# Optimization experiments

Hardware: AMD Instinct MI355X
Metric: run time of the kernel (lower is better)

## Reference

```python
import jax, jax.numpy as jnp
import numpy as np


def _dft_mats(N1, N):
    # Symmetric N1xN1 DFT / iDFT matrices and Cooley-Tukey twiddle factors.
    n = np.arange(N1)
    F = np.exp(-2j * np.pi * np.outer(n, n) / N1).astype(np.complex64)
    Finv = np.conj(F)  # inverse DFT matrix (1/N normalization folded into tw)
    tw = (np.exp(-2j * np.pi * np.outer(n, n) / N) / N).astype(np.complex64)
    twinv = np.exp(2j * np.pi * np.outer(n, n) / N).astype(np.complex64)
    return F, Finv, tw, twinv


def setup_inputs() -> dict:
    key = jax.random.key(0)
    ku, kk = jax.random.split(key)
    B, H, N = 128, 128, 1024
    u = jax.random.normal(ku, (B, H, N), dtype=jnp.float32)
    k = jax.random.normal(kk, (H, N), dtype=jnp.float32)
    return {"u": u, "k": k}


def reference(u, k):
    # Four-step (Monarch / Cooley-Tukey) FFT convolution: y = ifft(fft(u) * fft(k)).real
    # decomposed into N1xN1 complex matmuls with twiddle multiplies, matching TKFFTConv.
    B, H, N = u.shape
    N1 = int(round(np.sqrt(N)))
    F, Finv, tw, twinv = map(jnp.asarray, _dft_mats(N1, N))

    # Filter spectrum, reshaped (k2, k1) then transposed -> (H, k1, k2), as in __init__.
    kf = jnp.fft.fft(k, n=N)                              # (H, N) complex64
    kfT = jnp.swapaxes(kf.reshape(H, N1, N1), -1, -2)     # (H, k1, k2)

    x = u.reshape(B, H, N1, N1).astype(jnp.complex64)     # (B, H, n1, n2)
    x = jnp.einsum('kn,bhnm->bhkm', F, x)                 # DFT over n1 -> (k1, n2)
    x = x * tw                                            # twiddle (includes 1/N)
    x = jnp.einsum('bhkn,nl->bhkl', x, F)                 # DFT over n2 -> (k1, k2)
    x = x * kfT[None]                                     # pointwise filter in freq
    x = jnp.einsum('bhkl,ln->bhkn', x, Finv)              # iDFT over k2 -> (k1, n2)
    x = x * twinv                                         # inverse twiddle
    x = jnp.einsum('nk,bhkm->bhnm', Finv, x)              # iDFT over k1 -> (n1, n2)
    return x.real.reshape(B, H, N)
```

## Files before the change

### kernel.cpp

```cpp
#include <hip/hip_runtime.h>
#include <hip/hip_bf16.h>
#include <math.h>

typedef __attribute__((ext_vector_type(8))) short short8;
typedef __attribute__((ext_vector_type(16))) float f32x16;

union U {
    unsigned u[4];
    short8 s;
};

struct FragH {
    U f[2];
};

static __device__ __forceinline__ unsigned short f2bf(float x) {
    __bf16 b = (__bf16)x;
    return __builtin_bit_cast(unsigned short, b);
}
static __device__ __forceinline__ unsigned packbf(float a, float b) {
    return (unsigned)f2bf(a) | ((unsigned)f2bf(b) << 16);
}

#define MFMA(A, B, C) __builtin_amdgcn_mfma_f32_32x32x16_bf16((A).s, (B).s, (C), 0, 0, 0)


__global__ __launch_bounds__(256) void fft_tables(float2* tabs, float2* T1, uint4* Ftab) {
    int gid = blockIdx.x * 256 + threadIdx.x;
    if (gid < 1024) {
        int i = gid;
        int r = i >> 5, c = i & 31;
        float s32, c32;
        sincospif((float)((r * c) & 31) / 16.0f, &s32, &c32);
        s32 = -s32;
        tabs[i]        = make_float2(c32,  s32);
        tabs[1024 + i] = make_float2(c32, -s32);
        float sN, cN;
        sincospif((float)(r * c) / 512.0f, &sN, &cN);
        sN = -sN;
        tabs[2048 + i] = make_float2(cN / 1024.0f, sN / 1024.0f);
        tabs[3072 + i] = make_float2(cN, -sN);
        int m = i >> 6, l = i & 63;
        int row = (m & 3) + 8 * (m >> 2) + 4 * (l >> 5);
        int prod = (l & 31) * row;
        float st, ct;
        sincospif((float)prod / 512.0f, &st, &ct);
        T1[i] = make_float2(ct, -st);
    }
    if (gid < 1536) {
        int c = gid >> 9;
        int rem = gid & 511;
        int t = rem >> 8;
        int sub = rem & 255;
        int l = sub >> 2;
        int v = sub & 3;
        int k0 = 16 * t + 8 * (l >> 5) + 2 * v;
        int j = l & 31;
        unsigned short sh[2];
        for (int q = 0; q < 2; q++) {
            int k = k0 + q;
            float sa, ca;
            sincospif((float)((k * j) & 31) / 16.0f, &sa, &ca);
            float base = (c == 0) ? ca : ((c == 1) ? -sa : sa);
            sh[q] = f2bf(base);
        }
        ((unsigned*)Ftab)[((c * 2 + t) * 64 + l) * 4 + v] =
            (unsigned)sh[0] | ((unsigned)sh[1] << 16);
    }
}

__global__ __launch_bounds__(256) void kf_kernel(const float* __restrict__ kin,
                                                 const float2* __restrict__ tabs,
                                                 float2* __restrict__ kf_cd) {
    __shared__ float  sx[1024];
    __shared__ float2 sA[1024];
    const int h = blockIdx.x, t = threadIdx.x;
    for (int i = t; i < 1024; i += 256) sx[i] = kin[h * 1024 + i];
    __syncthreads();
    const int r = t >> 3, c0 = (t & 7) << 2;

    float2 acc[4];
    for (int j = 0; j < 4; j++) acc[j] = make_float2(0.f, 0.f);
    #pragma unroll 8
    for (int n1 = 0; n1 < 32; n1++) {
        float2 f = tabs[r * 32 + n1];
        for (int j = 0; j < 4; j++) {
            float xv = sx[n1 * 32 + c0 + j];
            acc[j].x += f.x * xv;
            acc[j].y += f.y * xv;
        }
    }
    for (int j = 0; j < 4; j++) {
        float2 w = tabs[3072 + r * 32 + c0 + j];
        sA[r * 32 + c0 + j] = make_float2(acc[j].x * w.x + acc[j].y * w.y,
                                          acc[j].y * w.x - acc[j].x * w.y);
    }
    __syncthreads();
    for (int j = 0; j < 4; j++) acc[j] = make_float2(0.f, 0.f);
    #pragma unroll 8
    for (int n2 = 0; n2 < 32; n2++) {
        float2 a = sA[r * 32 + n2];
        for (int j = 0; j < 4; j++) {
            float2 f = tabs[n2 * 32 + c0 + j];
            acc[j].x += a.x * f.x - a.y * f.y;
            acc[j].y += a.x * f.y + a.y * f.x;
        }
    }
    for (int j = 0; j < 4; j++) {
        int k2 = c0 + j;
        int m = (k2 & 3) | ((k2 >> 3) << 2);
        int hl = (k2 >> 2) & 1;
        kf_cd[h * 1024 + m * 64 + hl * 32 + r] =
            make_float2(acc[j].x * (1.0f / 1024.0f), acc[j].y * (1.0f / 1024.0f));
    }
}

static __device__ __forceinline__ void convertP(const f32x16& acc, FragH& out) {
    #pragma unroll
    for (int t = 0; t < 2; t++) {
        unsigned a0 = packbf(acc[8 * t + 0], acc[8 * t + 1]);
        unsigned a1 = packbf(acc[8 * t + 2], acc[8 * t + 3]);
        unsigned b0 = packbf(acc[8 * t + 4], acc[8 * t + 5]);
        unsigned b1 = packbf(acc[8 * t + 6], acc[8 * t + 7]);
        asm("v_permlane32_swap_b32 %0, %1" : "+v"(a0), "+v"(b0));
        asm("v_permlane32_swap_b32 %0, %1" : "+v"(a1), "+v"(b1));
        out.f[t].u[0] = a0;
        out.f[t].u[1] = a1;
        out.f[t].u[2] = b0;
        out.f[t].u[3] = b1;
    }
}

__global__ __launch_bounds__(256, 3) void conv_mfma(const float* __restrict__ u,
                                                    const float2* __restrict__ T1,
                                                    const uint4* __restrict__ Ftab,
                                                    const float2* __restrict__ KF,
                                                    float* __restrict__ out) {
    __shared__ float  sIO[8 * 1024];
    __shared__ float2 sT1[1024];
    __shared__ float2 sKF[1024];

    const int tid = threadIdx.x;
    const int lane = tid & 63;
    const int wave = tid >> 6;
    const int col = lane & 31;
    const int hl = lane >> 5;

    const int h = blockIdx.x >> 4;
    const int bblk = (blockIdx.x & 15) * 8;

    #pragma unroll
    for (int j = 0; j < 8; j++) {
        const float4* src = (const float4*)(u + ((size_t)((bblk + j) * 128 + h) << 10));
        *(float4*)&sIO[j * 1024 + tid * 4] = src[tid];
    }
    for (int i = tid; i < 1024; i += 256) {
        sT1[i] = T1[i];
        sKF[i] = KF[h * 1024 + i];
    }

    U F[3][2];
    #pragma unroll
    for (int c = 0; c < 3; c++)
        #pragma unroll
        for (int t = 0; t < 2; t++) {
            uint4 raw = Ftab[(c * 2 + t) * 64 + lane];
            F[c][t].u[0] = raw.x; F[c][t].u[1] = raw.y;
            F[c][t].u[2] = raw.z; F[c][t].u[3] = raw.w;
        }
    __syncthreads();

    const int tR = wave * 2, tI = wave * 2 + 1;
    U Xr[2], Xi[2];
    #pragma unroll
    for (int t = 0; t < 2; t++)
        #pragma unroll
        for (int v = 0; v < 4; v++) {
            int r0 = (16 * t + 8 * hl + 2 * v) * 32 + col;
            Xr[t].u[v] = packbf(sIO[tR * 1024 + r0], sIO[tR * 1024 + r0 + 32]);
            Xi[t].u[v] = packbf(sIO[tI * 1024 + r0], sIO[tI * 1024 + r0 + 32]);
        }

    const f32x16 Z16 = {0,0,0,0,0,0,0,0,0,0,0,0,0,0,0,0};

    f32x16 aR = Z16, aI = Z16;
    #pragma unroll
    for (int t = 0; t < 2; t++) {
        aR = MFMA(Xr[t], F[0][t], aR); aR = MFMA(Xi[t], F[2][t], aR);
        aI = MFMA(Xr[t], F[1][t], aI); aI = MFMA(Xi[t], F[0][t], aI);
    }
    #pragma unroll
    for (int m = 0; m < 16; m++) {
        float2 tm = sT1[m * 64 + lane];
        float rr = aR[m] * tm.x - aI[m] * tm.y;
        float ii = aR[m] * tm.y + aI[m] * tm.x;
        aR[m] = rr; aI[m] = ii;
    }
    FragH Yr, Yi;
    convertP(aR, Yr);
    convertP(aI, Yi);

    f32x16 bR = Z16, bI = Z16;
    #pragma unroll
    for (int t = 0; t < 2; t++) {
        bR = MFMA(F[0][t], Yr.f[t], bR); bR = MFMA(F[2][t], Yi.f[t], bR);
        bI = MFMA(F[0][t], Yi.f[t], bI); bI = MFMA(F[1][t], Yr.f[t], bI);
    }
    #pragma unroll
    for (int m = 0; m < 16; m++) {
        float2 kv = sKF[m * 64 + lane];
        float rr = bR[m] * kv.x - bI[m] * kv.y;
        float ii = bR[m] * kv.y + bI[m] * kv.x;
        bR[m] = rr; bI[m] = ii;
    }
    FragH Zr, Zi;
    convertP(bR, Zr);
    convertP(bI, Zi);

    aR = Z16; aI = Z16;
    #pragma unroll
    for (int t = 0; t < 2; t++) {
        aR = MFMA(Zr.f[t], F[0][t], aR); aR = MFMA(Zi.f[t], F[1][t], aR);
        aI = MFMA(Zr.f[t], F[2][t], aI); aI = MFMA(Zi.f[t], F[0][t], aI);
    }
    #pragma unroll
    for (int m = 0; m < 16; m++) {
        float2 tm = sT1[m * 64 + lane];
        float rr = aR[m] * tm.x + aI[m] * tm.y;
        float ii = aI[m] * tm.x - aR[m] * tm.y;
        aR[m] = rr; aI[m] = ii;
    }
    FragH Wr, Wi;
    convertP(aR, Wr);
    convertP(aI, Wi);

    f32x16 yR = Z16, yI = Z16;
    #pragma unroll
    for (int t = 0; t < 2; t++) {
        yR = MFMA(F[0][t], Wr.f[t], yR); yR = MFMA(F[1][t], Wi.f[t], yR);
        yI = MFMA(F[0][t], Wi.f[t], yI); yI = MFMA(F[2][t], Wr.f[t], yI);
    }

    #pragma unroll
    for (int m = 0; m < 16; m++) {
        int off = ((m & 3) + 8 * (m >> 2) + 4 * hl) * 32 + col;
        sIO[tR * 1024 + off] = yR[m];
        sIO[tI * 1024 + off] = yI[m];
    }
    __syncthreads();

    #pragma unroll
    for (int j = 0; j < 8; j++) {
        float4* dst = (float4*)(out + ((size_t)((bblk + j) * 128 + h) << 10));
        dst[tid] = *(const float4*)&sIO[j * 1024 + tid * 4];
    }
}

extern "C" void kernel_launch(void* const* d_in, const int* in_sizes, int n_in,
                              void* d_out, int out_size, void* d_ws, size_t ws_size,
                              hipStream_t stream) {
    const float* u = (const float*)d_in[0];
    const float* k = (const float*)d_in[1];
    float* out = (float*)d_out;

    float2* tabs  = (float2*)d_ws;
    float2* T1    = (float2*)((char*)d_ws + 32768);
    uint4*  Ftab  = (uint4*)((char*)d_ws + 49152);
    float2* kf_cd = (float2*)((char*)d_ws + 65536);

    fft_tables<<<16, 256, 0, stream>>>(tabs, T1, Ftab);
    kf_kernel<<<128, 256, 0, stream>>>(k, tabs, kf_cd);
    conv_mfma<<<2048, 256, 0, stream>>>(u, T1, Ftab, kf_cd, out);
}
```

Measured before the change: 46.11 us.

## Fuse table generation and filter FFT into single conv kernel with direct global IO

Removes the separate table and filter-spectrum kernels: each block computes twiddles and DFT fragments with sincospif, and runs the filter FFT through MFMA in-kernel for its head. The main kernel drops the shared-memory staging buffer and reads and writes u/out directly from global memory in fragment layout, with each wave processing two batch pairs. This cuts two launches and shared-memory traffic, at the cost of redundant per-block trig and filter work, uncoalesced strided global accesses, and a bf16-precision filter spectrum.

```diff
diff --git a/kernel.cpp b/kernel.cpp
--- a/kernel.cpp
+++ b/kernel.cpp
@@ -23,97 +23,6 @@
 }
 
 #define MFMA(A, B, C) __builtin_amdgcn_mfma_f32_32x32x16_bf16((A).s, (B).s, (C), 0, 0, 0)
-
-
-__global__ __launch_bounds__(256) void fft_tables(float2* tabs, float2* T1, uint4* Ftab) {
-    int gid = blockIdx.x * 256 + threadIdx.x;
-    if (gid < 1024) {
-        int i = gid;
-        int r = i >> 5, c = i & 31;
-        float s32, c32;
-        sincospif((float)((r * c) & 31) / 16.0f, &s32, &c32);
-        s32 = -s32;
-        tabs[i]        = make_float2(c32,  s32);
-        tabs[1024 + i] = make_float2(c32, -s32);
-        float sN, cN;
-        sincospif((float)(r * c) / 512.0f, &sN, &cN);
-        sN = -sN;
-        tabs[2048 + i] = make_float2(cN / 1024.0f, sN / 1024.0f);
-        tabs[3072 + i] = make_float2(cN, -sN);
-        int m = i >> 6, l = i & 63;
-        int row = (m & 3) + 8 * (m >> 2) + 4 * (l >> 5);
-        int prod = (l & 31) * row;
-        float st, ct;
-        sincospif((float)prod / 512.0f, &st, &ct);
-        T1[i] = make_float2(ct, -st);
-    }
-    if (gid < 1536) {
-        int c = gid >> 9;
-        int rem = gid & 511;
-        int t = rem >> 8;
-        int sub = rem & 255;
-        int l = sub >> 2;
-        int v = sub & 3;
-        int k0 = 16 * t + 8 * (l >> 5) + 2 * v;
-        int j = l & 31;
-        unsigned short sh[2];
-        for (int q = 0; q < 2; q++) {
-            int k = k0 + q;
-            float sa, ca;
-            sincospif((float)((k * j) & 31) / 16.0f, &sa, &ca);
-            float base = (c == 0) ? ca : ((c == 1) ? -sa : sa);
-            sh[q] = f2bf(base);
-        }
-        ((unsigned*)Ftab)[((c * 2 + t) * 64 + l) * 4 + v] =
-            (unsigned)sh[0] | ((unsigned)sh[1] << 16);
-    }
-}
-
-__global__ __launch_bounds__(256) void kf_kernel(const float* __restrict__ kin,
-                                                 const float2* __restrict__ tabs,
-                                                 float2* __restrict__ kf_cd) {
-    __shared__ float  sx[1024];
-    __shared__ float2 sA[1024];
-    const int h = blockIdx.x, t = threadIdx.x;
-    for (int i = t; i < 1024; i += 256) sx[i] = kin[h * 1024 + i];
-    __syncthreads();
-    const int r = t >> 3, c0 = (t & 7) << 2;
-
-    float2 acc[4];
-    for (int j = 0; j < 4; j++) acc[j] = make_float2(0.f, 0.f);
-    #pragma unroll 8
-    for (int n1 = 0; n1 < 32; n1++) {
-        float2 f = tabs[r * 32 + n1];
-        for (int j = 0; j < 4; j++) {
-            float xv = sx[n1 * 32 + c0 + j];
-            acc[j].x += f.x * xv;
-            acc[j].y += f.y * xv;
-        }
-    }
-    for (int j = 0; j < 4; j++) {
-        float2 w = tabs[3072 + r * 32 + c0 + j];
-        sA[r * 32 + c0 + j] = make_float2(acc[j].x * w.x + acc[j].y * w.y,
-                                          acc[j].y * w.x - acc[j].x * w.y);
-    }
-    __syncthreads();
-    for (int j = 0; j < 4; j++) acc[j] = make_float2(0.f, 0.f);
-    #pragma unroll 8
-    for (int n2 = 0; n2 < 32; n2++) {
-        float2 a = sA[r * 32 + n2];
-        for (int j = 0; j < 4; j++) {
-            float2 f = tabs[n2 * 32 + c0 + j];
-            acc[j].x += a.x * f.x - a.y * f.y;
-            acc[j].y += a.x * f.y + a.y * f.x;
-        }
-    }
-    for (int j = 0; j < 4; j++) {
-        int k2 = c0 + j;
-        int m = (k2 & 3) | ((k2 >> 3) << 2);
-        int hl = (k2 >> 2) & 1;
-        kf_cd[h * 1024 + m * 64 + hl * 32 + r] =
-            make_float2(acc[j].x * (1.0f / 1024.0f), acc[j].y * (1.0f / 1024.0f));
-    }
-}
 
 static __device__ __forceinline__ void convertP(const f32x16& acc, FragH& out) {
     #pragma unroll
@@ -131,12 +40,9 @@
     }
 }
 
-__global__ __launch_bounds__(256, 3) void conv_mfma(const float* __restrict__ u,
-                                                    const float2* __restrict__ T1,
-                                                    const uint4* __restrict__ Ftab,
-                                                    const float2* __restrict__ KF,
-                                                    float* __restrict__ out) {
-    __shared__ float  sIO[8 * 1024];
+__global__ __launch_bounds__(256, 3) void conv_all(const float* __restrict__ u,
+                                                   const float* __restrict__ kin,
+                                                   float* __restrict__ out) {
     __shared__ float2 sT1[1024];
     __shared__ float2 sKF[1024];
 
@@ -145,114 +51,156 @@
     const int wave = tid >> 6;
     const int col = lane & 31;
     const int hl = lane >> 5;
-
-    const int h = blockIdx.x >> 4;
-    const int bblk = (blockIdx.x & 15) * 8;
-
-    #pragma unroll
-    for (int j = 0; j < 8; j++) {
-        const float4* src = (const float4*)(u + ((size_t)((bblk + j) * 128 + h) << 10));
-        *(float4*)&sIO[j * 1024 + tid * 4] = src[tid];
-    }
+    const size_t tile_stride = (size_t)128 * 1024;
+
+    const int p0 = blockIdx.x * 8 + wave * 2;
+    const int h = blockIdx.x >> 3;
+
     for (int i = tid; i < 1024; i += 256) {
-        sT1[i] = T1[i];
-        sKF[i] = KF[h * 1024 + i];
+        int m = i >> 6, l = i & 63;
+        int row = (m & 3) + 8 * (m >> 2) + 4 * (l >> 5);
+        int prod = (l & 31) * row;
+        float st, ct;
+        sincospif((float)prod / 512.0f, &st, &ct);
+        sT1[i] = make_float2(ct, -st);
     }
 
     U F[3][2];
     #pragma unroll
-    for (int c = 0; c < 3; c++)
-        #pragma unroll
-        for (int t = 0; t < 2; t++) {
-            uint4 raw = Ftab[(c * 2 + t) * 64 + lane];
-            F[c][t].u[0] = raw.x; F[c][t].u[1] = raw.y;
-            F[c][t].u[2] = raw.z; F[c][t].u[3] = raw.w;
+    for (int t = 0; t < 2; t++)
+        #pragma unroll
+        for (int v = 0; v < 4; v++) {
+            float sa0, ca0, sa1, ca1;
+            int k0 = 16 * t + 8 * hl + 2 * v;
+            sincospif((float)((k0 * col) & 31) / 16.0f, &sa0, &ca0);
+            sincospif((float)(((k0 + 1) * col) & 31) / 16.0f, &sa1, &ca1);
+            F[0][t].u[v] = packbf(ca0, ca1);
+            F[1][t].u[v] = packbf(-sa0, -sa1);
+            F[2][t].u[v] = packbf(sa0, sa1);
         }
     __syncthreads();
 
-    const int tR = wave * 2, tI = wave * 2 + 1;
-    U Xr[2], Xi[2];
-    #pragma unroll
-    for (int t = 0; t < 2; t++)
-        #pragma unroll
-        for (int v = 0; v < 4; v++) {
-            int r0 = (16 * t + 8 * hl + 2 * v) * 32 + col;
-            Xr[t].u[v] = packbf(sIO[tR * 1024 + r0], sIO[tR * 1024 + r0 + 32]);
-            Xi[t].u[v] = packbf(sIO[tI * 1024 + r0], sIO[tI * 1024 + r0 + 32]);
-        }
-
     const f32x16 Z16 = {0,0,0,0,0,0,0,0,0,0,0,0,0,0,0,0};
 
-    f32x16 aR = Z16, aI = Z16;
-    #pragma unroll
-    for (int t = 0; t < 2; t++) {
-        aR = MFMA(Xr[t], F[0][t], aR); aR = MFMA(Xi[t], F[2][t], aR);
-        aI = MFMA(Xr[t], F[1][t], aI); aI = MFMA(Xi[t], F[0][t], aI);
-    }
-    #pragma unroll
-    for (int m = 0; m < 16; m++) {
-        float2 tm = sT1[m * 64 + lane];
-        float rr = aR[m] * tm.x - aI[m] * tm.y;
-        float ii = aR[m] * tm.y + aI[m] * tm.x;
-        aR[m] = rr; aI[m] = ii;
-    }
-    FragH Yr, Yi;
-    convertP(aR, Yr);
-    convertP(aI, Yi);
-
-    f32x16 bR = Z16, bI = Z16;
-    #pragma unroll
-    for (int t = 0; t < 2; t++) {
-        bR = MFMA(F[0][t], Yr.f[t], bR); bR = MFMA(F[2][t], Yi.f[t], bR);
-        bI = MFMA(F[0][t], Yi.f[t], bI); bI = MFMA(F[1][t], Yr.f[t], bI);
-    }
-    #pragma unroll
-    for (int m = 0; m < 16; m++) {
-        float2 kv = sKF[m * 64 + lane];
-        float rr = bR[m] * kv.x - bI[m] * kv.y;
-        float ii = bR[m] * kv.y + bI[m] * kv.x;
-        bR[m] = rr; bI[m] = ii;
-    }
-    FragH Zr, Zi;
-    convertP(bR, Zr);
-    convertP(bI, Zi);
-
-    aR = Z16; aI = Z16;
-    #pragma unroll
-    for (int t = 0; t < 2; t++) {
-        aR = MFMA(Zr.f[t], F[0][t], aR); aR = MFMA(Zi.f[t], F[1][t], aR);
-        aI = MFMA(Zr.f[t], F[2][t], aI); aI = MFMA(Zi.f[t], F[0][t], aI);
-    }
-    #pragma unroll
-    for (int m = 0; m < 16; m++) {
-        float2 tm = sT1[m * 64 + lane];
-        float rr = aR[m] * tm.x + aI[m] * tm.y;
-        float ii = aI[m] * tm.x - aR[m] * tm.y;
-        aR[m] = rr; aI[m] = ii;
-    }
-    FragH Wr, Wi;
-    convertP(aR, Wr);
-    convertP(aI, Wi);
-
-    f32x16 yR = Z16, yI = Z16;
-    #pragma unroll
-    for (int t = 0; t < 2; t++) {
-        yR = MFMA(F[0][t], Wr.f[t], yR); yR = MFMA(F[1][t], Wi.f[t], yR);
-        yI = MFMA(F[0][t], Wi.f[t], yI); yI = MFMA(F[2][t], Wr.f[t], yI);
-    }
-
-    #pragma unroll
-    for (int m = 0; m < 16; m++) {
-        int off = ((m & 3) + 8 * (m >> 2) + 4 * hl) * 32 + col;
-        sIO[tR * 1024 + off] = yR[m];
-        sIO[tI * 1024 + off] = yI[m];
+    {
+        const float* kp = kin + ((size_t)h << 10);
+        U Kr[2];
+        #pragma unroll
+        for (int t = 0; t < 2; t++)
+            #pragma unroll
+            for (int v = 0; v < 4; v++) {
+                int r0 = (16 * t + 8 * hl + 2 * v) * 32 + col;
+                Kr[t].u[v] = packbf(kp[r0], kp[r0 + 32]);
+            }
+        f32x16 aR = Z16, aI = Z16;
+        #pragma unroll
+        for (int t = 0; t < 2; t++) {
+            aR = MFMA(Kr[t], F[0][t], aR);
+            aI = MFMA(Kr[t], F[1][t], aI);
+        }
+        #pragma unroll
+        for (int m = 0; m < 16; m++) {
+            float2 tm = sT1[m * 64 + lane];
+            float rr = aR[m] * tm.x - aI[m] * tm.y;
+            float ii = aR[m] * tm.y + aI[m] * tm.x;
+            aR[m] = rr; aI[m] = ii;
+        }
+        FragH Yr, Yi;
+        convertP(aR, Yr);
+        convertP(aI, Yi);
+        f32x16 bR = Z16, bI = Z16;
+        #pragma unroll
+        for (int t = 0; t < 2; t++) {
+            bR = MFMA(F[0][t], Yr.f[t], bR); bR = MFMA(F[2][t], Yi.f[t], bR);
+            bI = MFMA(F[0][t], Yi.f[t], bI); bI = MFMA(F[1][t], Yr.f[t], bI);
+        }
+        #pragma unroll
+        for (int m = 0; m < 16; m++)
+            sKF[m * 64 + lane] = make_float2(bR[m] * (1.0f / 1024.0f),
+                                             bI[m] * (1.0f / 1024.0f));
     }
     __syncthreads();
 
-    #pragma unroll
-    for (int j = 0; j < 8; j++) {
-        float4* dst = (float4*)(out + ((size_t)((bblk + j) * 128 + h) << 10));
-        dst[tid] = *(const float4*)&sIO[j * 1024 + tid * 4];
+    for (int j = 0; j < 2; j++) {
+        const int b0 = ((p0 + j) & 63) * 2;
+        const float* upr = u + ((size_t)(b0 * 128 + h) << 10);
+        const float* upi = upr + tile_stride;
+
+        U Xr[2], Xi[2];
+        #pragma unroll
+        for (int t = 0; t < 2; t++)
+            #pragma unroll
+            for (int v = 0; v < 4; v++) {
+                int r0 = (16 * t + 8 * hl + 2 * v) * 32 + col;
+                Xr[t].u[v] = packbf(upr[r0], upr[r0 + 32]);
+                Xi[t].u[v] = packbf(upi[r0], upi[r0 + 32]);
+            }
+
+        f32x16 aR = Z16, aI = Z16;
+        #pragma unroll
+        for (int t = 0; t < 2; t++) {
+            aR = MFMA(Xr[t], F[0][t], aR); aR = MFMA(Xi[t], F[2][t], aR);
+            aI = MFMA(Xr[t], F[1][t], aI); aI = MFMA(Xi[t], F[0][t], aI);
+        }
+        #pragma unroll
+        for (int m = 0; m < 16; m++) {
+            float2 tm = sT1[m * 64 + lane];
+            float rr = aR[m] * tm.x - aI[m] * tm.y;
+            float ii = aR[m] * tm.y + aI[m] * tm.x;
+            aR[m] = rr; aI[m] = ii;
+        }
+        FragH Yr, Yi;
+        convertP(aR, Yr);
+        convertP(aI, Yi);
+
+        f32x16 bR = Z16, bI = Z16;
+        #pragma unroll
+        for (int t = 0; t < 2; t++) {
+            bR = MFMA(F[0][t], Yr.f[t], bR); bR = MFMA(F[2][t], Yi.f[t], bR);
+            bI = MFMA(F[0][t], Yi.f[t], bI); bI = MFMA(F[1][t], Yr.f[t], bI);
+        }
+        #pragma unroll
+        for (int m = 0; m < 16; m++) {
+            float2 kv = sKF[m * 64 + lane];
+            float rr = bR[m] * kv.x - bI[m] * kv.y;
+            float ii = bR[m] * kv.y + bI[m] * kv.x;
+            bR[m] = rr; bI[m] = ii;
+        }
+        FragH Zr, Zi;
+        convertP(bR, Zr);
+        convertP(bI, Zi);
+
+        aR = Z16; aI = Z16;
+        #pragma unroll
+        for (int t = 0; t < 2; t++) {
+            aR = MFMA(Zr.f[t], F[0][t], aR); aR = MFMA(Zi.f[t], F[1][t], aR);
+            aI = MFMA(Zr.f[t], F[2][t], aI); aI = MFMA(Zi.f[t], F[0][t], aI);
+        }
+        #pragma unroll
+        for (int m = 0; m < 16; m++) {
+            float2 tm = sT1[m * 64 + lane];
+            float rr = aR[m] * tm.x + aI[m] * tm.y;
+            float ii = aI[m] * tm.x - aR[m] * tm.y;
+            aR[m] = rr; aI[m] = ii;
+        }
+        FragH Wr, Wi;
+        convertP(aR, Wr);
+        convertP(aI, Wi);
+
+        f32x16 yR = Z16, yI = Z16;
+        #pragma unroll
+        for (int t = 0; t < 2; t++) {
+            yR = MFMA(F[0][t], Wr.f[t], yR); yR = MFMA(F[1][t], Wi.f[t], yR);
+            yI = MFMA(F[0][t], Wi.f[t], yI); yI = MFMA(F[2][t], Wr.f[t], yI);
+        }
+        float* opr = out + ((size_t)(b0 * 128 + h) << 10);
+        float* opi = opr + tile_stride;
+        #pragma unroll
+        for (int m = 0; m < 16; m++) {
+            int off = ((m & 3) + 8 * (m >> 2) + 4 * hl) * 32 + col;
+            opr[off] = yR[m];
+            opi[off] = yI[m];
+        }
     }
 }
 
@@ -263,12 +211,5 @@
     const float* k = (const float*)d_in[1];
     float* out = (float*)d_out;
 
-    float2* tabs  = (float2*)d_ws;
-    float2* T1    = (float2*)((char*)d_ws + 32768);
-    uint4*  Ftab  = (uint4*)((char*)d_ws + 49152);
-    float2* kf_cd = (float2*)((char*)d_ws + 65536);
-
-    fft_tables<<<16, 256, 0, stream>>>(tabs, T1, Ftab);
-    kf_kernel<<<128, 256, 0, stream>>>(k, tabs, kf_cd);
-    conv_mfma<<<2048, 256, 0, stream>>>(u, T1, Ftab, kf_cd, out);
-}
+    conv_all<<<1024, 256, 0, stream>>>(u, k, out);
+}
```

After: 67.76 us. +46.9%, slower.
